# Kernel tuning notes

Hardware: AMD Instinct MI355X
Metric: run time of the kernel (lower is better)

## Reference

```python
import jax, jax.numpy as jnp
import numpy as np

B, CH, N = 4, 128, 4096
PC = CH // 2  # pos channels = 64


def setup_inputs() -> dict:
    key = jax.random.key(0)
    ks = jax.random.split(key, 6)
    s_p = 1.0 / np.sqrt(PC)
    s_v = 1.0 / np.sqrt(CH)
    return {
        "pos_bot": jax.random.normal(ks[0], (B, PC, N), dtype=jnp.float32),
        "corr_feats": jax.random.normal(ks[1], (B, CH, N), dtype=jnp.float32),
        "Wp": jax.random.uniform(ks[2], (PC, PC), jnp.float32, -s_p, s_p),
        "bp": jax.random.uniform(ks[3], (PC,), jnp.float32, -s_p, s_p),
        "Wv": jax.random.uniform(ks[4], (CH, CH), jnp.float32, -s_v, s_v),
        "bv": jax.random.uniform(ks[5], (CH,), jnp.float32, -s_v, s_v),
        "beta": jnp.asarray([1.0], dtype=jnp.float32),
    }


def reference(pos_bot, corr_feats, Wp, bp, Wv, bv, beta):
    # 1x1 Conv1d == per-position matmul over channels
    pos = jnp.einsum("oc,bcn->bon", Wp, pos_bot) + bp[None, :, None]      # [B,64,N]
    value = jnp.einsum("oc,bcn->bon", Wv, corr_feats) + bv[None, :, None]  # [B,128,N]

    x = jnp.transpose(pos, (0, 2, 1))  # [B,N,64]
    # squared euclidean pairwise distance: ||xi||^2 + ||xj||^2 - 2 xi.xj
    sq = jnp.sum(x * x, axis=-1)  # [B,N]
    d2 = sq[:, :, None] + sq[:, None, :] - 2.0 * jnp.einsum("bnd,bmd->bnm", x, x)
    d2 = jnp.maximum(d2, 0.0)
    kernel = jnp.exp(-d2 * beta[0])  # [B,N,N] Gaussian RBF

    equation_F = jnp.transpose(value, (0, 2, 1))  # [B,N,128]
    return kernel, equation_F
```

## Files before the change

kernel.cpp:

```cpp
#include <hip/hip_runtime.h>
#include <hip/hip_bf16.h>

typedef _Float16 f16x8 __attribute__((ext_vector_type(8)));
typedef _Float16 f16x4 __attribute__((ext_vector_type(4)));
typedef float    f32x4 __attribute__((ext_vector_type(4)));

constexpr int BB = 4;
constexpr int CH = 128;
constexpr int PC = 64;
constexpr int NN = 4096;

__global__ __launch_bounds__(256) void proj_kernel(
    const float* __restrict__ pos_bot,
    const float* __restrict__ corr,
    const float* __restrict__ Wp,
    const float* __restrict__ bp,
    const float* __restrict__ Wv,
    const float* __restrict__ bv,
    _Float16* __restrict__ xbuf,
    float*    __restrict__ sq,
    float*    __restrict__ eqF)
{
    const int tid  = threadIdx.x;
    const int wid  = tid >> 6;
    const int lane = tid & 63;
    const int l15  = lane & 15;
    const int lg   = lane >> 4;
    const int b    = blockIdx.y & 3;
    const int n    = blockIdx.x * 16 + l15;

    if ((blockIdx.y >> 2) == 0) {
        const int mt = wid;
        f16x8 wf[2], pb[2];
#pragma unroll
        for (int ks = 0; ks < 2; ++ks) {
            const float* wp = Wp + (mt * 16 + l15) * PC + ks * 32 + lg * 8;
            f32x4 w0 = *reinterpret_cast<const f32x4*>(wp);
            f32x4 w1 = *reinterpret_cast<const f32x4*>(wp + 4);
            f16x8 f;
#pragma unroll
            for (int e = 0; e < 4; ++e) { f[e] = (_Float16)w0[e]; f[e + 4] = (_Float16)w1[e]; }
            wf[ks] = f;
            f16x8 g;
#pragma unroll
            for (int e = 0; e < 8; ++e) {
                const int c = ks * 32 + lg * 8 + e;
                g[e] = (_Float16)pos_bot[((size_t)(b * PC + c)) * NN + n];
            }
            pb[ks] = g;
        }

        f32x4 acc = {0.f, 0.f, 0.f, 0.f};
        acc = __builtin_amdgcn_mfma_f32_16x16x32_f16(wf[0], pb[0], acc, 0, 0, 0);
        acc = __builtin_amdgcn_mfma_f32_16x16x32_f16(wf[1], pb[1], acc, 0, 0, 0);

        float partial = 0.f;
        f16x4 h4;
#pragma unroll
        for (int r = 0; r < 4; ++r) {
            const int o = mt * 16 + lg * 4 + r;
            const float v = acc[r] + bp[o];
            const _Float16 h = (_Float16)v;
            h4[r] = h;
            const float hf = (float)h;
            partial = fmaf(hf, hf, partial);
        }
        *reinterpret_cast<f16x4*>(xbuf + ((size_t)(b * NN + n)) * PC + mt * 16 + lg * 4) = h4;

        partial += __shfl_xor(partial, 16);
        partial += __shfl_xor(partial, 32);
        __shared__ float psum[4][16];
        if (lane < 16) psum[wid][l15] = partial;
        __syncthreads();
        if (tid < 16)
            sq[b * NN + blockIdx.x * 16 + tid] =
                psum[0][tid] + psum[1][tid] + psum[2][tid] + psum[3][tid];
        return;
    }

    f16x8 cb[4];
#pragma unroll
    for (int ks = 0; ks < 4; ++ks) {
        f16x8 g;
#pragma unroll
        for (int e = 0; e < 8; ++e) {
            const int c = ks * 32 + lg * 8 + e;
            g[e] = (_Float16)corr[((size_t)(b * CH + c)) * NN + n];
        }
        cb[ks] = g;
    }
#pragma unroll
    for (int half = 0; half < 2; ++half) {
        const int ot = wid + half * 4;
        f32x4 acc = {0.f, 0.f, 0.f, 0.f};
#pragma unroll
        for (int ks = 0; ks < 4; ++ks) {
            const float* wv = Wv + (ot * 16 + l15) * CH + ks * 32 + lg * 8;
            f32x4 w0 = *reinterpret_cast<const f32x4*>(wv);
            f32x4 w1 = *reinterpret_cast<const f32x4*>(wv + 4);
            f16x8 f;
#pragma unroll
            for (int e = 0; e < 4; ++e) { f[e] = (_Float16)w0[e]; f[e + 4] = (_Float16)w1[e]; }
            acc = __builtin_amdgcn_mfma_f32_16x16x32_f16(f, cb[ks], acc, 0, 0, 0);
        }
        f32x4 o4;
#pragma unroll
        for (int r = 0; r < 4; ++r) o4[r] = acc[r] + bv[ot * 16 + lg * 4 + r];
        __builtin_nontemporal_store(
            o4, reinterpret_cast<f32x4*>(eqF + ((size_t)(b * NN + n)) * CH + ot * 16 + lg * 4));
    }
}

__global__ __launch_bounds__(256) void gram_kernel(
    const _Float16* __restrict__ xbuf,
    const float*    __restrict__ sq,
    const float*    __restrict__ beta,
    float*          __restrict__ out)
{
    const int tid  = threadIdx.x;
    const int wid  = tid >> 6;
    const int lane = tid & 63;
    const int l15  = lane & 15;
    const int lg   = lane >> 4;
    const int b    = blockIdx.z;
    const int jb   = blockIdx.x * 512;
    const int rb   = blockIdx.y * 64;

    const _Float16* xb  = xbuf + (size_t)b * NN * PC;
    const float*    sqb = sq + (size_t)b * NN;

    const float bs   = -beta[0] * 1.44269504088896f;
    const float m2bs = -2.f * bs;

    f16x8 bf[8][2];
    float tj[8];
#pragma unroll
    for (int jtf = 0; jtf < 8; ++jtf) {
        const int j = jb + wid * 128 + jtf * 16 + l15;
#pragma unroll
        for (int ks = 0; ks < 2; ++ks)
            bf[jtf][ks] = *reinterpret_cast<const f16x8*>(
                xb + (size_t)j * PC + ks * 32 + lg * 8);
        tj[jtf] = bs * sqb[j];
    }

    __shared__ float lds[16][516];

    for (int sl = 0; sl < 4; ++sl) {
        const int ibase = rb + sl * 16;

        const f16x8 af0 = *reinterpret_cast<const f16x8*>(
            xb + (size_t)(ibase + l15) * PC + lg * 8);
        const f16x8 af1 = *reinterpret_cast<const f16x8*>(
            xb + (size_t)(ibase + l15) * PC + 32 + lg * 8);

        f32x4 acc[8];
#pragma unroll
        for (int jtf = 0; jtf < 8; ++jtf) {
            f32x4 z = {0.f, 0.f, 0.f, 0.f};
            acc[jtf] = __builtin_amdgcn_mfma_f32_16x16x32_f16(af0, bf[jtf][0], z, 0, 0, 0);
        }
#pragma unroll
        for (int jtf = 0; jtf < 8; ++jtf)
            acc[jtf] = __builtin_amdgcn_mfma_f32_16x16x32_f16(af1, bf[jtf][1], acc[jtf], 0, 0, 0);

        float ti[4];
#pragma unroll
        for (int r = 0; r < 4; ++r) ti[r] = bs * sqb[ibase + lg * 4 + r];

        if (sl) __syncthreads();

#pragma unroll
        for (int jtf = 0; jtf < 8; ++jtf) {
#pragma unroll
            for (int r = 0; r < 4; ++r) {
                float arg = fminf(fmaf(m2bs, acc[jtf][r], ti[r] + tj[jtf]), 0.f);
                lds[lg * 4 + r][wid * 128 + jtf * 16 + l15] =
                    __builtin_amdgcn_exp2f(arg);
            }
        }
        __syncthreads();

#pragma unroll
        for (int rr = 0; rr < 4; ++rr) {
            const int row = rr * 4 + wid;
            float* orow = out + ((size_t)(b * NN + ibase + row)) * NN + jb;
#pragma unroll
            for (int c2 = 0; c2 < 2; ++c2) {
                const int col = c2 * 256 + lane * 4;
                __builtin_nontemporal_store(
                    *reinterpret_cast<const f32x4*>(&lds[row][col]),
                    reinterpret_cast<f32x4*>(orow + col));
            }
        }
    }
}

extern "C" void kernel_launch(void* const* d_in, const int* in_sizes, int n_in,
                              void* d_out, int out_size, void* d_ws, size_t ws_size,
                              hipStream_t stream) {
    const float* pos_bot = (const float*)d_in[0];
    const float* corr    = (const float*)d_in[1];
    const float* Wp      = (const float*)d_in[2];
    const float* bp      = (const float*)d_in[3];
    const float* Wv      = (const float*)d_in[4];
    const float* bv      = (const float*)d_in[5];
    const float* beta    = (const float*)d_in[6];

    float* out = (float*)d_out;
    float* eqF = out + (size_t)BB * NN * NN;

    _Float16* xbuf = (_Float16*)d_ws;
    float* sq = (float*)((char*)d_ws + (size_t)BB * NN * PC * sizeof(_Float16));

    proj_kernel<<<dim3(NN / 16, 2 * BB), 256, 0, stream>>>(
        pos_bot, corr, Wp, bp, Wv, bv, xbuf, sq, eqF);

    gram_kernel<<<dim3(NN / 512, NN / 64, BB), 256, 0, stream>>>(
        xbuf, sq, beta, out);
}
```

Before: 70.62 us.

## Drop LDS staging in gram kernel and store RBF tiles directly from MFMA

Rewrites the Gram/RBF kernel to swap MFMA operands so each lane holds four consecutive output columns and stores them straight to global memory, removing the shared-memory transpose and its barriers. Blocks are remapped on a 1-D grid so that each XCD owns a contiguous range of rows, with each block covering a 256x128 tile split into four 128x64 wave tiles. The clamp of the exponent argument at zero is dropped. This risks less contiguous global writes per row and values slightly above 1 on the diagonal.

```diff
diff --git a/kernel.cpp b/kernel.cpp
--- a/kernel.cpp
+++ b/kernel.cpp
@@ -122,9 +122,18 @@
     const int lane = tid & 63;
     const int l15  = lane & 15;
     const int lg   = lane >> 4;
-    const int b    = blockIdx.z;
-    const int jb   = blockIdx.x * 512;
-    const int rb   = blockIdx.y * 64;
+
+    const int bid  = blockIdx.x;
+    const int xcd  = bid & 7;
+    const int k    = bid >> 3;
+    const int jt32 = k & 31;
+    const int i2   = (k >> 5) & 1;
+    const int b    = k >> 6;
+    const int ib   = xcd * 512 + i2 * 256;
+    const int jb   = jt32 * 128;
+
+    const int wib  = ib + (wid >> 1) * 128;
+    const int wjb  = jb + (wid & 1) * 64;
 
     const _Float16* xb  = xbuf + (size_t)b * NN * PC;
     const float*    sqb = sq + (size_t)b * NN;
@@ -132,66 +141,36 @@
     const float bs   = -beta[0] * 1.44269504088896f;
     const float m2bs = -2.f * bs;
 
-    f16x8 bf[8][2];
-    float tj[8];
+    f16x8 bf[4][2];
+    f32x4 tj[4];
 #pragma unroll
-    for (int jtf = 0; jtf < 8; ++jtf) {
-        const int j = jb + wid * 128 + jtf * 16 + l15;
+    for (int jt = 0; jt < 4; ++jt) {
 #pragma unroll
         for (int ks = 0; ks < 2; ++ks)
-            bf[jtf][ks] = *reinterpret_cast<const f16x8*>(
-                xb + (size_t)j * PC + ks * 32 + lg * 8);
-        tj[jtf] = bs * sqb[j];
+            bf[jt][ks] = *reinterpret_cast<const f16x8*>(
+                xb + (size_t)(wjb + jt * 16 + l15) * PC + ks * 32 + lg * 8);
+        f32x4 s = *reinterpret_cast<const f32x4*>(sqb + wjb + jt * 16 + lg * 4);
+        tj[jt] = s * bs;
     }
 
-    __shared__ float lds[16][516];
-
-    for (int sl = 0; sl < 4; ++sl) {
-        const int ibase = rb + sl * 16;
-
-        const f16x8 af0 = *reinterpret_cast<const f16x8*>(
-            xb + (size_t)(ibase + l15) * PC + lg * 8);
-        const f16x8 af1 = *reinterpret_cast<const f16x8*>(
-            xb + (size_t)(ibase + l15) * PC + 32 + lg * 8);
-
-        f32x4 acc[8];
-#pragma unroll
-        for (int jtf = 0; jtf < 8; ++jtf) {
-            f32x4 z = {0.f, 0.f, 0.f, 0.f};
-            acc[jtf] = __builtin_amdgcn_mfma_f32_16x16x32_f16(af0, bf[jtf][0], z, 0, 0, 0);
-        }
-#pragma unroll
-        for (int jtf = 0; jtf < 8; ++jtf)
-            acc[jtf] = __builtin_amdgcn_mfma_f32_16x16x32_f16(af1, bf[jtf][1], acc[jtf], 0, 0, 0);
-
-        float ti[4];
-#pragma unroll
-        for (int r = 0; r < 4; ++r) ti[r] = bs * sqb[ibase + lg * 4 + r];
-
-        if (sl) __syncthreads();
+    for (int it = 0; it < 8; ++it) {
+        const int i = wib + it * 16 + l15;
+        const f16x8 af0 = *reinterpret_cast<const f16x8*>(xb + (size_t)i * PC + lg * 8);
+        const f16x8 af1 = *reinterpret_cast<const f16x8*>(xb + (size_t)i * PC + 32 + lg * 8);
+        const float ti  = bs * sqb[i];
+        float* orow = out + ((size_t)(b * NN + i)) * NN + wjb;
 
 #pragma unroll
-        for (int jtf = 0; jtf < 8; ++jtf) {
+        for (int jt = 0; jt < 4; ++jt) {
+            f32x4 z = {0.f, 0.f, 0.f, 0.f};
+            f32x4 acc = __builtin_amdgcn_mfma_f32_16x16x32_f16(bf[jt][0], af0, z, 0, 0, 0);
+            acc = __builtin_amdgcn_mfma_f32_16x16x32_f16(bf[jt][1], af1, acc, 0, 0, 0);
+            f32x4 v;
 #pragma unroll
-            for (int r = 0; r < 4; ++r) {
-                float arg = fminf(fmaf(m2bs, acc[jtf][r], ti[r] + tj[jtf]), 0.f);
-                lds[lg * 4 + r][wid * 128 + jtf * 16 + l15] =
-                    __builtin_amdgcn_exp2f(arg);
-            }
-        }
-        __syncthreads();
-
-#pragma unroll
-        for (int rr = 0; rr < 4; ++rr) {
-            const int row = rr * 4 + wid;
-            float* orow = out + ((size_t)(b * NN + ibase + row)) * NN + jb;
-#pragma unroll
-            for (int c2 = 0; c2 < 2; ++c2) {
-                const int col = c2 * 256 + lane * 4;
-                __builtin_nontemporal_store(
-                    *reinterpret_cast<const f32x4*>(&lds[row][col]),
-                    reinterpret_cast<f32x4*>(orow + col));
-            }
+            for (int r = 0; r < 4; ++r)
+                v[r] = __builtin_amdgcn_exp2f(fmaf(m2bs, acc[r], ti + tj[jt][r]));
+            __builtin_nontemporal_store(
+                v, reinterpret_cast<f32x4*>(orow + jt * 16 + lg * 4));
         }
     }
 }
@@ -216,6 +195,5 @@
     proj_kernel<<<dim3(NN / 16, 2 * BB), 256, 0, stream>>>(
         pos_bot, corr, Wp, bp, Wv, bv, xbuf, sq, eqF);
 
-    gram_kernel<<<dim3(NN / 512, NN / 64, BB), 256, 0, stream>>>(
-        xbuf, sq, beta, out);
+    gram_kernel<<<dim3(2048), 256, 0, stream>>>(xbuf, sq, beta, out);
 }
```

Result: slower. 108.8 us (+54.1%).

## Give each wave a private LDS tile and drop block-wide barriers in gram kernel

Applied to the files above, without the earlier changes.

The gram kernel now keeps a separate 16x128 LDS staging tile for each wave, so every wave transposes and stores only its own columns and no __syncthreads is needed. The four per-row sq loads are also merged into one vector load. This removes block-wide barrier stalls between the exp compute and the store phase. In exchange each store now writes 512-byte row segments per wave instead of 2KB per row, and the code relies on same-wave LDS ordering without an explicit fence.

```diff
diff --git a/kernel.cpp b/kernel.cpp
--- a/kernel.cpp
+++ b/kernel.cpp
@@ -125,6 +125,7 @@
     const int b    = blockIdx.z;
     const int jb   = blockIdx.x * 512;
     const int rb   = blockIdx.y * 64;
+    const int wjb  = jb + wid * 128;
 
     const _Float16* xb  = xbuf + (size_t)b * NN * PC;
     const float*    sqb = sq + (size_t)b * NN;
@@ -136,7 +137,7 @@
     float tj[8];
 #pragma unroll
     for (int jtf = 0; jtf < 8; ++jtf) {
-        const int j = jb + wid * 128 + jtf * 16 + l15;
+        const int j = wjb + jtf * 16 + l15;
 #pragma unroll
         for (int ks = 0; ks < 2; ++ks)
             bf[jtf][ks] = *reinterpret_cast<const f16x8*>(
@@ -144,7 +145,7 @@
         tj[jtf] = bs * sqb[j];
     }
 
-    __shared__ float lds[16][516];
+    __shared__ float lds[4][16][132];
 
     for (int sl = 0; sl < 4; ++sl) {
         const int ibase = rb + sl * 16;
@@ -164,34 +165,26 @@
         for (int jtf = 0; jtf < 8; ++jtf)
             acc[jtf] = __builtin_amdgcn_mfma_f32_16x16x32_f16(af1, bf[jtf][1], acc[jtf], 0, 0, 0);
 
-        float ti[4];
-#pragma unroll
-        for (int r = 0; r < 4; ++r) ti[r] = bs * sqb[ibase + lg * 4 + r];
-
-        if (sl) __syncthreads();
+        const f32x4 sv = *reinterpret_cast<const f32x4*>(sqb + ibase + lg * 4);
 
 #pragma unroll
         for (int jtf = 0; jtf < 8; ++jtf) {
 #pragma unroll
             for (int r = 0; r < 4; ++r) {
-                float arg = fminf(fmaf(m2bs, acc[jtf][r], ti[r] + tj[jtf]), 0.f);
-                lds[lg * 4 + r][wid * 128 + jtf * 16 + l15] =
-                    __builtin_amdgcn_exp2f(arg);
+                const float ti = bs * sv[r];
+                float arg = fminf(fmaf(m2bs, acc[jtf][r], ti + tj[jtf]), 0.f);
+                lds[wid][lg * 4 + r][jtf * 16 + l15] = __builtin_amdgcn_exp2f(arg);
             }
         }
-        __syncthreads();
-
-#pragma unroll
-        for (int rr = 0; rr < 4; ++rr) {
-            const int row = rr * 4 + wid;
-            float* orow = out + ((size_t)(b * NN + ibase + row)) * NN + jb;
-#pragma unroll
-            for (int c2 = 0; c2 < 2; ++c2) {
-                const int col = c2 * 256 + lane * 4;
-                __builtin_nontemporal_store(
-                    *reinterpret_cast<const f32x4*>(&lds[row][col]),
-                    reinterpret_cast<f32x4*>(orow + col));
-            }
+
+#pragma unroll
+        for (int k = 0; k < 8; ++k) {
+            const int row = 2 * k + (lane >> 5);
+            const int col = (lane & 31) * 4;
+            const f32x4 v = *reinterpret_cast<const f32x4*>(&lds[wid][row][col]);
+            __builtin_nontemporal_store(
+                v, reinterpret_cast<f32x4*>(
+                       out + ((size_t)(b * NN + ibase + row)) * NN + wjb + col));
         }
     }
 }
```

Result: no change. 70.38 us (-0.3%).

## Make each gram block sweep a full 16-row stripe across all columns

Applied to the files above, without the earlier changes.

The gram kernel is reorganized so each block owns 16 rows and loops over all 4096 columns in 512-wide chunks, reloading the column operand each iteration. Before, each block kept a 512-column tile in registers and reused it across 64 rows. The new layout writes whole contiguous output rows per block and cuts the grid to 1024 blocks, but it rereads the column fragments far more often. It also adds a barrier every chunk. The output write of 256 MB dominates, so the change mostly affects the store access pattern and scheduling.

```diff
diff --git a/kernel.cpp b/kernel.cpp
--- a/kernel.cpp
+++ b/kernel.cpp
@@ -122,9 +122,8 @@
     const int lane = tid & 63;
     const int l15  = lane & 15;
     const int lg   = lane >> 4;
-    const int b    = blockIdx.z;
-    const int jb   = blockIdx.x * 512;
-    const int rb   = blockIdx.y * 64;
+    const int b    = blockIdx.y;
+    const int rb   = blockIdx.x * 16;
 
     const _Float16* xb  = xbuf + (size_t)b * NN * PC;
     const float*    sqb = sq + (size_t)b * NN;
@@ -132,27 +131,29 @@
     const float bs   = -beta[0] * 1.44269504088896f;
     const float m2bs = -2.f * bs;
 
-    f16x8 bf[8][2];
-    float tj[8];
-#pragma unroll
-    for (int jtf = 0; jtf < 8; ++jtf) {
-        const int j = jb + wid * 128 + jtf * 16 + l15;
-#pragma unroll
-        for (int ks = 0; ks < 2; ++ks)
-            bf[jtf][ks] = *reinterpret_cast<const f16x8*>(
-                xb + (size_t)j * PC + ks * 32 + lg * 8);
-        tj[jtf] = bs * sqb[j];
-    }
-
-    __shared__ float lds[16][516];
-
-    for (int sl = 0; sl < 4; ++sl) {
-        const int ibase = rb + sl * 16;
-
-        const f16x8 af0 = *reinterpret_cast<const f16x8*>(
-            xb + (size_t)(ibase + l15) * PC + lg * 8);
-        const f16x8 af1 = *reinterpret_cast<const f16x8*>(
-            xb + (size_t)(ibase + l15) * PC + 32 + lg * 8);
+    const f16x8 af0 = *reinterpret_cast<const f16x8*>(
+        xb + (size_t)(rb + l15) * PC + lg * 8);
+    const f16x8 af1 = *reinterpret_cast<const f16x8*>(
+        xb + (size_t)(rb + l15) * PC + 32 + lg * 8);
+    f32x4 tiv = *reinterpret_cast<const f32x4*>(sqb + rb + lg * 4);
+    tiv = tiv * bs;
+
+    __shared__ float ldsT[16][516];
+
+    for (int c = 0; c < 8; ++c) {
+        const int wjb = c * 512 + wid * 128;
+
+        f16x8 bf[8][2];
+        float tj[8];
+#pragma unroll
+        for (int jtf = 0; jtf < 8; ++jtf) {
+            const int j = wjb + jtf * 16 + l15;
+#pragma unroll
+            for (int ks = 0; ks < 2; ++ks)
+                bf[jtf][ks] = *reinterpret_cast<const f16x8*>(
+                    xb + (size_t)j * PC + ks * 32 + lg * 8);
+            tj[jtf] = bs * sqb[j];
+        }
 
         f32x4 acc[8];
 #pragma unroll
@@ -164,18 +165,14 @@
         for (int jtf = 0; jtf < 8; ++jtf)
             acc[jtf] = __builtin_amdgcn_mfma_f32_16x16x32_f16(af1, bf[jtf][1], acc[jtf], 0, 0, 0);
 
-        float ti[4];
-#pragma unroll
-        for (int r = 0; r < 4; ++r) ti[r] = bs * sqb[ibase + lg * 4 + r];
-
-        if (sl) __syncthreads();
+        __syncthreads();
 
 #pragma unroll
         for (int jtf = 0; jtf < 8; ++jtf) {
 #pragma unroll
             for (int r = 0; r < 4; ++r) {
-                float arg = fminf(fmaf(m2bs, acc[jtf][r], ti[r] + tj[jtf]), 0.f);
-                lds[lg * 4 + r][wid * 128 + jtf * 16 + l15] =
+                const float arg = fminf(fmaf(m2bs, acc[jtf][r], tiv[r] + tj[jtf]), 0.f);
+                ldsT[lg * 4 + r][wid * 128 + jtf * 16 + l15] =
                     __builtin_amdgcn_exp2f(arg);
             }
         }
@@ -183,14 +180,14 @@
 
 #pragma unroll
         for (int rr = 0; rr < 4; ++rr) {
-            const int row = rr * 4 + wid;
-            float* orow = out + ((size_t)(b * NN + ibase + row)) * NN + jb;
-#pragma unroll
-            for (int c2 = 0; c2 < 2; ++c2) {
-                const int col = c2 * 256 + lane * 4;
+            const int row = wid * 4 + rr;
+            float* dst = out + ((size_t)(b * NN + rb + row)) * NN + c * 512;
+#pragma unroll
+            for (int half = 0; half < 2; ++half) {
+                const int col = half * 256 + lane * 4;
                 __builtin_nontemporal_store(
-                    *reinterpret_cast<const f32x4*>(&lds[row][col]),
-                    reinterpret_cast<f32x4*>(orow + col));
+                    *reinterpret_cast<const f32x4*>(&ldsT[row][col]),
+                    reinterpret_cast<f32x4*>(dst + col));
             }
         }
     }
@@ -216,6 +213,5 @@
     proj_kernel<<<dim3(NN / 16, 2 * BB), 256, 0, stream>>>(
         pos_bot, corr, Wp, bp, Wv, bv, xbuf, sq, eqF);
 
-    gram_kernel<<<dim3(NN / 512, NN / 64, BB), 256, 0, stream>>>(
-        xbuf, sq, beta, out);
+    gram_kernel<<<dim3(NN / 16, BB), 256, 0, stream>>>(xbuf, sq, beta, out);
 }
```

New measurement: 97.48 us. 1.38x slower.
